# Performance work log

Measured on AMD Instinct MI355X. Metric: run time of the kernel, lower is better.

## Reference

```python
import jax, jax.numpy as jnp
import numpy as np

B, H, SEQLEN, HEAD_DIM = 1, 16, 4096, 64
SCALE = 1.0 / float(np.sqrt(HEAD_DIM))


def setup_inputs() -> dict:
    key = jax.random.key(0)
    kq, kk, kv = jax.random.split(key, 3)
    q = jax.random.normal(kq, (B, H, SEQLEN, HEAD_DIM), dtype=jnp.float32)
    k = jax.random.normal(kk, (B, H, HEAD_DIM, SEQLEN), dtype=jnp.float32)  # pre-transposed
    v = jax.random.normal(kv, (B, H, SEQLEN, HEAD_DIM), dtype=jnp.float32)
    return {"q": q, "k": k, "v": v}


def reference(q, k, v):
    # causal additive mask: -inf strictly above the diagonal
    mask = jnp.where(
        jnp.triu(jnp.ones((SEQLEN, SEQLEN), dtype=bool), k=1),
        jnp.float32(-jnp.inf), jnp.float32(0.0),
    ).astype(q.dtype)
    scores = jnp.einsum('bhsd,bhdt->bhst', q, k) * SCALE + mask  # [B,H,S,S]
    row_max = jnp.max(scores, axis=-1, keepdims=True)
    p_exp = jnp.exp(scores - row_max)
    denom = jnp.sum(p_exp, axis=-1, keepdims=True)
    p = p_exp / denom                                            # softmax probs
    out = jnp.einsum('bhst,bhtd->bhsd', p, v)                    # [B,H,S,D]
    row_sum = jnp.sum(p, axis=2)                                 # per-key accumulated attention [B,H,S]
    return (out, row_sum)
```

## Files before the change

### kernel.cpp

```cpp
#include <hip/hip_runtime.h>
#include <hip/hip_bf16.h>

#define HEADS 16
#define SEQ   4096
#define DIM   64
#define QT    64
#define KT    64
#define SCALE 0.125f
#define CF    0.18033688011112042f
#define LOG2E 1.4426950408889634f

typedef __bf16 v8bf  __attribute__((ext_vector_type(8)));
typedef __bf16 v4bf  __attribute__((ext_vector_type(4)));
typedef float  f32x4 __attribute__((ext_vector_type(4)));

__device__ __forceinline__ __bf16 to_bf(float f) { return (__bf16)f; }
__device__ __forceinline__ float ex2(float x) { return __builtin_amdgcn_exp2f(x); }
__device__ __forceinline__ float lg2(float x) { return __builtin_amdgcn_logf(x); }

__device__ __forceinline__ void gload16(const __bf16* g, __bf16* l) {
    __builtin_amdgcn_global_load_lds(
        (const __attribute__((address_space(1))) void*)g,
        (__attribute__((address_space(3))) void*)l,
        16, 0, 0);
}

__global__ __launch_bounds__(256) void conv_q_kernel(
    const float* __restrict__ qg, __bf16* __restrict__ Qb)
{
    size_t i = ((size_t)blockIdx.x * 256 + threadIdx.x) * 8;
    float4 f0 = *(const float4*)(qg + i);
    float4 f1 = *(const float4*)(qg + i + 4);
    v8bf o;
    o[0] = to_bf(f0.x * CF); o[1] = to_bf(f0.y * CF);
    o[2] = to_bf(f0.z * CF); o[3] = to_bf(f0.w * CF);
    o[4] = to_bf(f1.x * CF); o[5] = to_bf(f1.y * CF);
    o[6] = to_bf(f1.z * CF); o[7] = to_bf(f1.w * CF);
    *(v8bf*)(Qb + i) = o;
}

__global__ __launch_bounds__(256) void conv_kv_kernel(
    const float* __restrict__ kg, const float* __restrict__ vg,
    __bf16* __restrict__ Kb, __bf16* __restrict__ Vb)
{
    __shared__ __bf16 ldsT[64][65];
    const int h   = blockIdx.y;
    const int t0  = blockIdx.x * 64;
    const int tid = threadIdx.x;
    const int rr  = tid >> 2;
    const int cq  = (tid & 3) * 16;

    if (blockIdx.z == 0) {
        const float* src = kg + ((size_t)h * DIM + rr) * SEQ + t0 + cq;
        #pragma unroll
        for (int j = 0; j < 4; ++j) {
            float4 f = *(const float4*)(src + 4 * j);
            ldsT[rr][cq + 4 * j + 0] = to_bf(f.x);
            ldsT[rr][cq + 4 * j + 1] = to_bf(f.y);
            ldsT[rr][cq + 4 * j + 2] = to_bf(f.z);
            ldsT[rr][cq + 4 * j + 3] = to_bf(f.w);
        }
        __syncthreads();
        __bf16* dst = Kb + (size_t)h * SEQ * DIM + (size_t)(t0 + rr) * DIM + cq;
        v8bf o0, o1;
        #pragma unroll
        for (int i = 0; i < 8; ++i) {
            o0[i] = ldsT[cq + i][rr];
            o1[i] = ldsT[cq + 8 + i][rr];
        }
        *(v8bf*)dst = o0;
        *(v8bf*)(dst + 8) = o1;
    } else {
        const float* src = vg + ((size_t)h * SEQ + t0 + rr) * DIM + cq;
        #pragma unroll
        for (int j = 0; j < 4; ++j) {
            float4 f = *(const float4*)(src + 4 * j);
            ldsT[rr][cq + 4 * j + 0] = to_bf(f.x);
            ldsT[rr][cq + 4 * j + 1] = to_bf(f.y);
            ldsT[rr][cq + 4 * j + 2] = to_bf(f.z);
            ldsT[rr][cq + 4 * j + 3] = to_bf(f.w);
        }
        __syncthreads();
        __bf16* dst0 = Vb + ((size_t)h * DIM + rr) * SEQ + t0;
        const int n  = cq >> 4;
        const int c0 = 32 * (n >> 1) + 4 * (n & 1);
        #pragma unroll
        for (int j2 = 0; j2 < 4; ++j2) {
            v4bf ch;
            #pragma unroll
            for (int r = 0; r < 4; ++r)
                ch[r] = ldsT[cq + 4 * j2 + r][rr];
            *(v4bf*)(dst0 + c0 + 8 * j2) = ch;
        }
    }
}

__global__ __launch_bounds__(256, 2) void fa_fwd2_kernel(
    const __bf16* __restrict__ Qb, const __bf16* __restrict__ Kb,
    const __bf16* __restrict__ Vb, float* __restrict__ outg,
    float* __restrict__ lseg)
{
    const int b    = blockIdx.x;
    const int xcd  = b & 7;
    const int j    = b >> 3;
    const int h    = 2 * xcd + (j & 1);
    const int bq   = j >> 1;
    const int tid  = threadIdx.x;
    const int wave = tid >> 6;
    const int lane = tid & 63;
    const int g    = lane >> 4;
    const int l16  = lane & 15;

    __shared__ alignas(16) __bf16 ldsK[2][KT * DIM];
    __shared__ alignas(16) __bf16 ldsV[2][DIM * KT];

    const int r0 = tid >> 3;
    const int c0 = tid & 7;
    const size_t kOff0 = (size_t)r0 * DIM + (size_t)((c0 ^ (r0 & 7)) << 3);
    const size_t kOff1 = (size_t)(r0 + 32) * DIM + (size_t)((c0 ^ ((r0 + 32) & 7)) << 3);
    const size_t vOff0 = (size_t)r0 * SEQ + (size_t)((c0 ^ (r0 & 7)) << 3);
    const size_t vOff1 = (size_t)(r0 + 32) * SEQ + (size_t)((c0 ^ ((r0 + 32) & 7)) << 3);
    const __bf16* KbH = Kb + (size_t)h * SEQ * DIM;
    const __bf16* VbH = Vb + (size_t)h * DIM * SEQ;
    const int ldsW = wave * 512;

    #pragma unroll 1
    for (int pi = 0; pi < 2; ++pi) {
        const int qtile = pi ? (63 - bq) : bq;
        const int qw = qtile * QT + wave * 16;
        const int nt = qtile + 1;
        const int q  = qw + l16;

        const __bf16* qrow = Qb + ((size_t)h * SEQ + q) * DIM + g * 8;
        v8bf aq0 = *(const v8bf*)qrow;
        v8bf aq1 = *(const v8bf*)(qrow + 32);

        f32x4 acc[4];
        #pragma unroll
        for (int n = 0; n < 4; ++n) acc[n] = (f32x4){0.f, 0.f, 0.f, 0.f};
        float lp[4] = {0.f, 0.f, 0.f, 0.f};

        int cur = 0;
        gload16(KbH + kOff0, &ldsK[0][ldsW]);
        gload16(KbH + kOff1, &ldsK[0][2048 + ldsW]);
        gload16(VbH + vOff0, &ldsV[0][ldsW]);
        gload16(VbH + vOff1, &ldsV[0][2048 + ldsW]);
        __syncthreads();

        #pragma unroll 1
        for (int t = 0; t < nt; ++t) {
            if (t + 1 < nt) {
                const size_t kt = (size_t)(t + 1) * KT * DIM;
                const size_t vt = (size_t)(t + 1) * KT;
                gload16(KbH + kt + kOff0, &ldsK[cur ^ 1][ldsW]);
                gload16(KbH + kt + kOff1, &ldsK[cur ^ 1][2048 + ldsW]);
                gload16(VbH + vt + vOff0, &ldsV[cur ^ 1][ldsW]);
                gload16(VbH + vt + vOff1, &ldsV[cur ^ 1][2048 + ldsW]);
            }
            f32x4 s[4];
            #pragma unroll
            for (int n = 0; n < 4; ++n) s[n] = (f32x4){0.f, 0.f, 0.f, 0.f};
            __builtin_amdgcn_s_setprio(1);
            #pragma unroll
            for (int kk = 0; kk < 2; ++kk) {
                #pragma unroll
                for (int n = 0; n < 4; ++n) {
                    int row  = 16 * n + l16;
                    int byte = row * 128 + kk * 64 + g * 16;
                    byte ^= (row & 7) << 4;
                    v8bf ak = *(const v8bf*)&ldsK[cur][byte >> 1];
                    s[n] = __builtin_amdgcn_mfma_f32_16x16x32_bf16(
                        ak, kk ? aq1 : aq0, s[n], 0, 0, 0);
                }
            }
            __builtin_amdgcn_s_setprio(0);
            if (t == nt - 1) {
                const int qit = wave * 16 + l16;
                #pragma unroll
                for (int n = 0; n < 4; ++n)
                    #pragma unroll
                    for (int r = 0; r < 4; ++r)
                        if (16 * n + 4 * g + r > qit) s[n][r] = -3.0e38f;
            }
            v8bf pa0, pa1;
            #pragma unroll
            for (int n = 0; n < 4; ++n) {
                #pragma unroll
                for (int r = 0; r < 4; ++r) {
                    float p = ex2(s[n][r]);
                    lp[r] += p;
                    if (n < 2) pa0[(n & 1) * 4 + r] = to_bf(p);
                    else       pa1[(n & 1) * 4 + r] = to_bf(p);
                }
            }
            __builtin_amdgcn_s_setprio(1);
            #pragma unroll
            for (int kk = 0; kk < 2; ++kk) {
                #pragma unroll
                for (int n = 0; n < 4; ++n) {
                    int row  = 16 * n + l16;
                    int byte = row * 128 + kk * 64 + g * 16;
                    byte ^= (row & 7) << 4;
                    v8bf av = *(const v8bf*)&ldsV[cur][byte >> 1];
                    acc[n] = __builtin_amdgcn_mfma_f32_16x16x32_bf16(
                        av, kk ? pa1 : pa0, acc[n], 0, 0, 0);
                }
            }
            __builtin_amdgcn_s_setprio(0);
            __syncthreads();
            cur ^= 1;
        }

        float l = (lp[0] + lp[1]) + (lp[2] + lp[3]);
        l += __shfl_xor(l, 16);
        l += __shfl_xor(l, 32);
        const float inv = 1.0f / l;
        float* orow = outg + ((size_t)h * SEQ + q) * DIM;
        #pragma unroll
        for (int n = 0; n < 4; ++n) {
            f32x4 o = acc[n];
            o[0] *= inv; o[1] *= inv; o[2] *= inv; o[3] *= inv;
            *(f32x4*)(orow + 16 * n + 4 * g) = o;
        }
        if (g == 0)
            lseg[h * SEQ + q] = lg2(l);
    }
}

__global__ __launch_bounds__(256, 2) void fa_colsum2_kernel(
    const __bf16* __restrict__ Qb, const __bf16* __restrict__ Kb,
    const float* __restrict__ lseg, float* __restrict__ rsg)
{
    const int b    = blockIdx.x;
    const int xcd  = b & 7;
    const int j    = b >> 3;
    const int h    = 2 * xcd + (j & 1);
    const int ta   = j >> 1;
    const int tb   = 63 - ta;
    const int tid  = threadIdx.x;
    const int wave = tid >> 6;
    const int lane = tid & 63;
    const int g    = lane >> 4;
    const int l16  = lane & 15;

    __shared__ alignas(16) __bf16 ldsK2[2][KT * DIM];
    __shared__ float cs[2][4][KT];

    const int r0 = tid >> 3;
    const int c0 = tid & 7;
    const size_t kOff0 = (size_t)r0 * DIM + (size_t)((c0 ^ (r0 & 7)) << 3);
    const size_t kOff1 = (size_t)(r0 + 32) * DIM + (size_t)((c0 ^ ((r0 + 32) & 7)) << 3);
    const __bf16* KbH = Kb + (size_t)h * SEQ * DIM;
    const int ldsW = wave * 512;

    gload16(KbH + (size_t)ta * KT * DIM + kOff0, &ldsK2[0][ldsW]);
    gload16(KbH + (size_t)ta * KT * DIM + kOff1, &ldsK2[0][2048 + ldsW]);
    gload16(KbH + (size_t)tb * KT * DIM + kOff0, &ldsK2[1][ldsW]);
    gload16(KbH + (size_t)tb * KT * DIM + kOff1, &ldsK2[1][2048 + ldsW]);
    __syncthreads();

    float accA[4] = {0.f, 0.f, 0.f, 0.f};
    float accB[4] = {0.f, 0.f, 0.f, 0.f};

    #pragma unroll 1
    for (int qt = ta; qt < SEQ / QT; ++qt) {
        const int qw = qt * QT + wave * 16;
        const __bf16* qrow = Qb + ((size_t)h * SEQ + qw + l16) * DIM + g * 8;
        v8bf aq0 = *(const v8bf*)qrow;
        v8bf aq1 = *(const v8bf*)(qrow + 32);
        float4 lse4 = *(const float4*)(lseg + (size_t)h * SEQ + qw + 4 * g);

        {
            f32x4 s[4];
            #pragma unroll
            for (int n = 0; n < 4; ++n) s[n] = (f32x4){0.f, 0.f, 0.f, 0.f};
            __builtin_amdgcn_s_setprio(1);
            #pragma unroll
            for (int kk = 0; kk < 2; ++kk)
                #pragma unroll
                for (int n = 0; n < 4; ++n) {
                    int row  = 16 * n + l16;
                    int byte = row * 128 + kk * 64 + g * 16;
                    byte ^= (row & 7) << 4;
                    v8bf bk = *(const v8bf*)&ldsK2[0][byte >> 1];
                    s[n] = __builtin_amdgcn_mfma_f32_16x16x32_bf16(
                        kk ? aq1 : aq0, bk, s[n], 0, 0, 0);
                }
            __builtin_amdgcn_s_setprio(0);
            if (qt == ta) {
                #pragma unroll
                for (int n = 0; n < 4; ++n) {
                    const int key = ta * KT + 16 * n + l16;
                    #pragma unroll
                    for (int r = 0; r < 4; ++r) {
                        float e = ex2(s[n][r] - lse4[r]);
                        accA[n] += (key <= qw + 4 * g + r) ? e : 0.f;
                    }
                }
            } else {
                #pragma unroll
                for (int n = 0; n < 4; ++n)
                    #pragma unroll
                    for (int r = 0; r < 4; ++r)
                        accA[n] += ex2(s[n][r] - lse4[r]);
            }
        }
        if (qt >= tb) {
            f32x4 s[4];
            #pragma unroll
            for (int n = 0; n < 4; ++n) s[n] = (f32x4){0.f, 0.f, 0.f, 0.f};
            __builtin_amdgcn_s_setprio(1);
            #pragma unroll
            for (int kk = 0; kk < 2; ++kk)
                #pragma unroll
                for (int n = 0; n < 4; ++n) {
                    int row  = 16 * n + l16;
                    int byte = row * 128 + kk * 64 + g * 16;
                    byte ^= (row & 7) << 4;
                    v8bf bk = *(const v8bf*)&ldsK2[1][byte >> 1];
                    s[n] = __builtin_amdgcn_mfma_f32_16x16x32_bf16(
                        kk ? aq1 : aq0, bk, s[n], 0, 0, 0);
                }
            __builtin_amdgcn_s_setprio(0);
            if (qt == tb) {
                #pragma unroll
                for (int n = 0; n < 4; ++n) {
                    const int key = tb * KT + 16 * n + l16;
                    #pragma unroll
                    for (int r = 0; r < 4; ++r) {
                        float e = ex2(s[n][r] - lse4[r]);
                        accB[n] += (key <= qw + 4 * g + r) ? e : 0.f;
                    }
                }
            } else {
                #pragma unroll
                for (int n = 0; n < 4; ++n)
                    #pragma unroll
                    for (int r = 0; r < 4; ++r)
                        accB[n] += ex2(s[n][r] - lse4[r]);
            }
        }
    }

    #pragma unroll
    for (int n = 0; n < 4; ++n) {
        accA[n] += __shfl_xor(accA[n], 16);
        accA[n] += __shfl_xor(accA[n], 32);
        accB[n] += __shfl_xor(accB[n], 16);
        accB[n] += __shfl_xor(accB[n], 32);
    }
    if (lane < 16) {
        #pragma unroll
        for (int n = 0; n < 4; ++n) {
            cs[0][wave][16 * n + lane] = accA[n];
            cs[1][wave][16 * n + lane] = accB[n];
        }
    }
    __syncthreads();
    if (tid < KT) {
        rsg[(size_t)h * SEQ + ta * KT + tid] =
            cs[0][0][tid] + cs[0][1][tid] + cs[0][2][tid] + cs[0][3][tid];
    } else if (tid < 2 * KT) {
        const int t = tid - KT;
        rsg[(size_t)h * SEQ + tb * KT + t] =
            cs[1][0][t] + cs[1][1][t] + cs[1][2][t] + cs[1][3][t];
    }
}

__global__ __launch_bounds__(256, 1) void fa_fwd_v1_kernel(
    const float* __restrict__ qg, const float* __restrict__ kg,
    const float* __restrict__ vg, float* __restrict__ outg,
    float* __restrict__ lseg)
{
    const int h    = blockIdx.y;
    const int q0   = blockIdx.x * QT;
    const int tid  = threadIdx.x;
    const int wave = tid >> 6;
    const int lane = tid & 63;
    const int g    = lane >> 4;
    const int l16  = lane & 15;

    __shared__ alignas(16) __bf16 ldsK[KT * DIM];
    __shared__ alignas(16) __bf16 ldsV[DIM * KT];
    __shared__ alignas(16) __bf16 ldsP[4][16 * 72];

    const int qw = q0 + wave * 16;
    v8bf aq[2];
    {
        const float* qrow = qg + ((size_t)h * SEQ + qw + l16) * DIM;
        #pragma unroll
        for (int kk = 0; kk < 2; ++kk) {
            const float* p = qrow + kk * 32 + g * 8;
            float4 f0 = *(const float4*)p;
            float4 f1 = *(const float4*)(p + 4);
            aq[kk][0] = to_bf(f0.x); aq[kk][1] = to_bf(f0.y);
            aq[kk][2] = to_bf(f0.z); aq[kk][3] = to_bf(f0.w);
            aq[kk][4] = to_bf(f1.x); aq[kk][5] = to_bf(f1.y);
            aq[kk][6] = to_bf(f1.z); aq[kk][7] = to_bf(f1.w);
        }
    }
    f32x4 acc[4];
    #pragma unroll
    for (int n = 0; n < 4; ++n) acc[n] = (f32x4){0.f, 0.f, 0.f, 0.f};
    float m_r[4], l_r[4];
    #pragma unroll
    for (int r = 0; r < 4; ++r) { m_r[r] = -__builtin_inff(); l_r[r] = 0.f; }

    const int ntiles = q0 / KT + 1;
    const int kd = tid >> 2;
    const int kc = (tid & 3) * 16;

    for (int t = 0; t < ntiles; ++t) {
        const int t0 = t * KT;
        __syncthreads();
        {
            const float* src = kg + ((size_t)h * DIM + kd) * SEQ + t0 + kc;
            #pragma unroll
            for (int j = 0; j < 4; ++j) {
                float4 f = *(const float4*)(src + 4 * j);
                #pragma unroll
                for (int i = 0; i < 4; ++i) {
                    int row  = kc + 4 * j + i;
                    int byte = row * 128 + kd * 2;
                    byte ^= (row & 7) << 4;
                    ldsK[byte >> 1] = to_bf(((const float*)&f)[i]);
                }
            }
        }
        {
            const float* src = vg + ((size_t)h * SEQ + t0 + kd) * DIM + kc;
            #pragma unroll
            for (int j = 0; j < 4; ++j) {
                float4 f = *(const float4*)(src + 4 * j);
                #pragma unroll
                for (int i = 0; i < 4; ++i) {
                    int row  = kc + 4 * j + i;
                    int byte = row * 128 + kd * 2;
                    byte ^= (row & 7) << 4;
                    ldsV[byte >> 1] = to_bf(((const float*)&f)[i]);
                }
            }
        }
        __syncthreads();

        f32x4 s[4];
        #pragma unroll
        for (int n = 0; n < 4; ++n) s[n] = (f32x4){0.f, 0.f, 0.f, 0.f};
        #pragma unroll
        for (int kk = 0; kk < 2; ++kk)
            #pragma unroll
            for (int n = 0; n < 4; ++n) {
                int row  = 16 * n + l16;
                int byte = row * 128 + kk * 64 + g * 16;
                byte ^= (row & 7) << 4;
                v8bf bk = *(const v8bf*)&ldsK[byte >> 1];
                s[n] = __builtin_amdgcn_mfma_f32_16x16x32_bf16(aq[kk], bk, s[n], 0, 0, 0);
            }
        float pvv[4][4];
        #pragma unroll
        for (int r = 0; r < 4; ++r) {
            const int qq = qw + 4 * g + r;
            float sv[4];
            #pragma unroll
            for (int n = 0; n < 4; ++n) {
                int key = t0 + 16 * n + l16;
                sv[n] = (key <= qq) ? s[n][r] * (SCALE * LOG2E) : -3.0e38f;
            }
            float mx = fmaxf(fmaxf(sv[0], sv[1]), fmaxf(sv[2], sv[3]));
            mx = fmaxf(mx, __shfl_xor(mx, 1));
            mx = fmaxf(mx, __shfl_xor(mx, 2));
            mx = fmaxf(mx, __shfl_xor(mx, 4));
            mx = fmaxf(mx, __shfl_xor(mx, 8));
            float mnew = fmaxf(m_r[r], mx);
            float corr = ex2(m_r[r] - mnew);
            m_r[r] = mnew;
            float rs = 0.f;
            #pragma unroll
            for (int n = 0; n < 4; ++n) {
                float p = (sv[n] > -1.0e38f) ? ex2(sv[n] - mnew) : 0.f;
                pvv[n][r] = p;
                rs += p;
            }
            rs += __shfl_xor(rs, 1);
            rs += __shfl_xor(rs, 2);
            rs += __shfl_xor(rs, 4);
            rs += __shfl_xor(rs, 8);
            l_r[r] = l_r[r] * corr + rs;
            #pragma unroll
            for (int n = 0; n < 4; ++n) acc[n][r] *= corr;
        }
        #pragma unroll
        for (int n = 0; n < 4; ++n)
            #pragma unroll
            for (int r = 0; r < 4; ++r)
                ldsP[wave][(4 * g + r) * 72 + 16 * n + l16] = to_bf(pvv[n][r]);
        asm volatile("s_waitcnt lgkmcnt(0)" ::: "memory");
        __builtin_amdgcn_sched_barrier(0);
        #pragma unroll
        for (int kk = 0; kk < 2; ++kk) {
            v8bf ap = *(const v8bf*)&ldsP[wave][l16 * 72 + 32 * kk + 8 * g];
            #pragma unroll
            for (int n = 0; n < 4; ++n) {
                int row  = 16 * n + l16;
                int byte = row * 128 + kk * 64 + g * 16;
                byte ^= (row & 7) << 4;
                v8bf bv = *(const v8bf*)&ldsV[byte >> 1];
                acc[n] = __builtin_amdgcn_mfma_f32_16x16x32_bf16(ap, bv, acc[n], 0, 0, 0);
            }
        }
    }
    #pragma unroll
    for (int r = 0; r < 4; ++r) {
        const int qq  = qw + 4 * g + r;
        const float inv = 1.0f / l_r[r];
        float* orow = outg + ((size_t)h * SEQ + qq) * DIM;
        #pragma unroll
        for (int n = 0; n < 4; ++n)
            orow[16 * n + l16] = acc[n][r] * inv;
        if (l16 == 0)
            lseg[h * SEQ + qq] = m_r[r] + lg2(l_r[r]);
    }
}

__global__ __launch_bounds__(256, 1) void fa_colsum_v1_kernel(
    const float* __restrict__ qg, const float* __restrict__ kg,
    const float* __restrict__ lseg, float* __restrict__ rsg)
{
    const int h    = blockIdx.y;
    const int t0   = blockIdx.x * KT;
    const int tid  = threadIdx.x;
    const int wave = tid >> 6;
    const int lane = tid & 63;
    const int g    = lane >> 4;
    const int l16  = lane & 15;

    __shared__ alignas(16) __bf16 ldsK[KT * DIM];
    __shared__ float cs[4][KT];
    {
        const int kd = tid >> 2;
        const int kc = (tid & 3) * 16;
        const float* src = kg + ((size_t)h * DIM + kd) * SEQ + t0 + kc;
        #pragma unroll
        for (int j = 0; j < 4; ++j) {
            float4 f = *(const float4*)(src + 4 * j);
            #pragma unroll
            for (int i = 0; i < 4; ++i) {
                int row  = kc + 4 * j + i;
                int byte = row * 128 + kd * 2;
                byte ^= (row & 7) << 4;
                ldsK[byte >> 1] = to_bf(((const float*)&f)[i]);
            }
        }
    }
    __syncthreads();
    float colacc[4] = {0.f, 0.f, 0.f, 0.f};
    for (int qt = t0 / QT; qt < SEQ / QT; ++qt) {
        const int qw = qt * QT + wave * 16;
        const float* qrow = qg + ((size_t)h * SEQ + qw + l16) * DIM;
        v8bf aq[2];
        #pragma unroll
        for (int kk = 0; kk < 2; ++kk) {
            const float* p = qrow + kk * 32 + g * 8;
            float4 f0 = *(const float4*)p;
            float4 f1 = *(const float4*)(p + 4);
            aq[kk][0] = to_bf(f0.x); aq[kk][1] = to_bf(f0.y);
            aq[kk][2] = to_bf(f0.z); aq[kk][3] = to_bf(f0.w);
            aq[kk][4] = to_bf(f1.x); aq[kk][5] = to_bf(f1.y);
            aq[kk][6] = to_bf(f1.z); aq[kk][7] = to_bf(f1.w);
        }
        float lse_r[4];
        #pragma unroll
        for (int r = 0; r < 4; ++r)
            lse_r[r] = lseg[h * SEQ + qw + 4 * g + r];
        f32x4 s[4];
        #pragma unroll
        for (int n = 0; n < 4; ++n) s[n] = (f32x4){0.f, 0.f, 0.f, 0.f};
        #pragma unroll
        for (int kk = 0; kk < 2; ++kk)
            #pragma unroll
            for (int n = 0; n < 4; ++n) {
                int row  = 16 * n + l16;
                int byte = row * 128 + kk * 64 + g * 16;
                byte ^= (row & 7) << 4;
                v8bf bk = *(const v8bf*)&ldsK[byte >> 1];
                s[n] = __builtin_amdgcn_mfma_f32_16x16x32_bf16(aq[kk], bk, s[n], 0, 0, 0);
            }
        #pragma unroll
        for (int n = 0; n < 4; ++n) {
            const int key = t0 + 16 * n + l16;
            #pragma unroll
            for (int r = 0; r < 4; ++r) {
                const int qq = qw + 4 * g + r;
                if (key <= qq)
                    colacc[n] += ex2(s[n][r] * (SCALE * LOG2E) - lse_r[r]);
            }
        }
    }
    #pragma unroll
    for (int n = 0; n < 4; ++n) {
        colacc[n] += __shfl_xor(colacc[n], 16);
        colacc[n] += __shfl_xor(colacc[n], 32);
    }
    if (lane < 16) {
        #pragma unroll
        for (int n = 0; n < 4; ++n)
            cs[wave][16 * n + lane] = colacc[n];
    }
    __syncthreads();
    if (tid < KT) {
        float v = cs[0][tid] + cs[1][tid] + cs[2][tid] + cs[3][tid];
        rsg[h * SEQ + t0 + tid] = v;
    }
}

extern "C" void kernel_launch(void* const* d_in, const int* in_sizes, int n_in,
                              void* d_out, int out_size, void* d_ws, size_t ws_size,
                              hipStream_t stream) {
    (void)in_sizes; (void)n_in; (void)out_size;
    const float* qg = (const float*)d_in[0];
    const float* kg = (const float*)d_in[1];
    const float* vg = (const float*)d_in[2];
    float* outg = (float*)d_out;
    float* rsg  = outg + (size_t)HEADS * SEQ * DIM;

    const size_t nElem   = (size_t)HEADS * SEQ * DIM;
    const size_t lseB    = (size_t)HEADS * SEQ * sizeof(float);
    const size_t needB   = lseB + 3 * nElem * sizeof(__bf16);

    if (ws_size >= needB) {
        float*  lseg = (float*)d_ws;
        __bf16* Qb = (__bf16*)((char*)d_ws + lseB);
        __bf16* Kb = Qb + nElem;
        __bf16* Vb = Kb + nElem;
        conv_q_kernel<<<dim3((int)(nElem / 2048)), 256, 0, stream>>>(qg, Qb);
        conv_kv_kernel<<<dim3(SEQ / 64, HEADS, 2), 256, 0, stream>>>(kg, vg, Kb, Vb);
        fa_fwd2_kernel<<<dim3(512), 256, 0, stream>>>(Qb, Kb, Vb, outg, lseg);
        fa_colsum2_kernel<<<dim3(512), 256, 0, stream>>>(Qb, Kb, lseg, rsg);
    } else {
        float* lseg = (float*)d_ws;
        dim3 grid(SEQ / QT, HEADS);
        fa_fwd_v1_kernel<<<grid, 256, 0, stream>>>(qg, kg, vg, outg, lseg);
        fa_colsum_v1_kernel<<<grid, 256, 0, stream>>>(qg, kg, lseg, rsg);
    }
}
```

Measured before the change: 117.8 us.

## Process two 64-key KV tiles per loop iteration in forward attention

Each main-loop iteration of the forward kernel now loads and consumes two 64-wide K/V tiles (128 keys) instead of one. The LDS buffers gain an extra dimension to match. This halves the number of barriers and loop trips and gives the scheduler two independent MFMA chains to interleave. In exchange it doubles LDS use per block and adds register pressure. When the tile count is odd, the last iteration also computes a fully masked extra tile, which is wasted work.

Result: faster. 105.3 us (-10.6%).

```diff
diff --git a/kernel.cpp b/kernel.cpp
--- a/kernel.cpp
+++ b/kernel.cpp
@@ -111,8 +111,8 @@
     const int g    = lane >> 4;
     const int l16  = lane & 15;
 
-    __shared__ alignas(16) __bf16 ldsK[2][KT * DIM];
-    __shared__ alignas(16) __bf16 ldsV[2][DIM * KT];
+    __shared__ alignas(16) __bf16 ldsK[2][2][KT * DIM];
+    __shared__ alignas(16) __bf16 ldsV[2][2][DIM * KT];
 
     const int r0 = tid >> 3;
     const int c0 = tid & 7;
@@ -128,8 +128,9 @@
     for (int pi = 0; pi < 2; ++pi) {
         const int qtile = pi ? (63 - bq) : bq;
         const int qw = qtile * QT + wave * 16;
-        const int nt = qtile + 1;
-        const int q  = qw + l16;
+        const int nt  = qtile + 1;
+        const int nIt = (nt + 1) >> 1;
+        const int q   = qw + l16;
 
         const __bf16* qrow = Qb + ((size_t)h * SEQ + q) * DIM + g * 8;
         v8bf aq0 = *(const v8bf*)qrow;
@@ -141,25 +142,36 @@
         float lp[4] = {0.f, 0.f, 0.f, 0.f};
 
         int cur = 0;
-        gload16(KbH + kOff0, &ldsK[0][ldsW]);
-        gload16(KbH + kOff1, &ldsK[0][2048 + ldsW]);
-        gload16(VbH + vOff0, &ldsV[0][ldsW]);
-        gload16(VbH + vOff1, &ldsV[0][2048 + ldsW]);
+        #pragma unroll
+        for (int u = 0; u < 2; ++u) {
+            const __bf16* kb = KbH + (size_t)(64 * u) * DIM;
+            const __bf16* vb = VbH + 64 * u;
+            gload16(kb + kOff0, &ldsK[0][u][ldsW]);
+            gload16(kb + kOff1, &ldsK[0][u][2048 + ldsW]);
+            gload16(vb + vOff0, &ldsV[0][u][ldsW]);
+            gload16(vb + vOff1, &ldsV[0][u][2048 + ldsW]);
+        }
         __syncthreads();
 
         #pragma unroll 1
-        for (int t = 0; t < nt; ++t) {
-            if (t + 1 < nt) {
-                const size_t kt = (size_t)(t + 1) * KT * DIM;
-                const size_t vt = (size_t)(t + 1) * KT;
-                gload16(KbH + kt + kOff0, &ldsK[cur ^ 1][ldsW]);
-                gload16(KbH + kt + kOff1, &ldsK[cur ^ 1][2048 + ldsW]);
-                gload16(VbH + vt + vOff0, &ldsV[cur ^ 1][ldsW]);
-                gload16(VbH + vt + vOff1, &ldsV[cur ^ 1][2048 + ldsW]);
-            }
-            f32x4 s[4];
-            #pragma unroll
-            for (int n = 0; n < 4; ++n) s[n] = (f32x4){0.f, 0.f, 0.f, 0.f};
+        for (int it = 0; it < nIt; ++it) {
+            if (it + 1 < nIt) {
+                #pragma unroll
+                for (int u = 0; u < 2; ++u) {
+                    const __bf16* kb = KbH + (size_t)(128 * (it + 1) + 64 * u) * DIM;
+                    const __bf16* vb = VbH + 128 * (it + 1) + 64 * u;
+                    gload16(kb + kOff0, &ldsK[cur ^ 1][u][ldsW]);
+                    gload16(kb + kOff1, &ldsK[cur ^ 1][u][2048 + ldsW]);
+                    gload16(vb + vOff0, &ldsV[cur ^ 1][u][ldsW]);
+                    gload16(vb + vOff1, &ldsV[cur ^ 1][u][2048 + ldsW]);
+                }
+            }
+            f32x4 s0[4], s1[4];
+            #pragma unroll
+            for (int n = 0; n < 4; ++n) {
+                s0[n] = (f32x4){0.f, 0.f, 0.f, 0.f};
+                s1[n] = (f32x4){0.f, 0.f, 0.f, 0.f};
+            }
             __builtin_amdgcn_s_setprio(1);
             #pragma unroll
             for (int kk = 0; kk < 2; ++kk) {
@@ -168,29 +180,44 @@
                     int row  = 16 * n + l16;
                     int byte = row * 128 + kk * 64 + g * 16;
                     byte ^= (row & 7) << 4;
-                    v8bf ak = *(const v8bf*)&ldsK[cur][byte >> 1];
-                    s[n] = __builtin_amdgcn_mfma_f32_16x16x32_bf16(
-                        ak, kk ? aq1 : aq0, s[n], 0, 0, 0);
+                    v8bf ak0 = *(const v8bf*)&ldsK[cur][0][byte >> 1];
+                    v8bf ak1 = *(const v8bf*)&ldsK[cur][1][byte >> 1];
+                    s0[n] = __builtin_amdgcn_mfma_f32_16x16x32_bf16(
+                        ak0, kk ? aq1 : aq0, s0[n], 0, 0, 0);
+                    s1[n] = __builtin_amdgcn_mfma_f32_16x16x32_bf16(
+                        ak1, kk ? aq1 : aq0, s1[n], 0, 0, 0);
                 }
             }
             __builtin_amdgcn_s_setprio(0);
-            if (t == nt - 1) {
-                const int qit = wave * 16 + l16;
+            const int st0 = 2 * it, st1 = 2 * it + 1;
+            if (st0 >= nt - 1) {
+                const int lim = (qtile - st0) * 64 + wave * 16 + l16;
                 #pragma unroll
                 for (int n = 0; n < 4; ++n)
                     #pragma unroll
                     for (int r = 0; r < 4; ++r)
-                        if (16 * n + 4 * g + r > qit) s[n][r] = -3.0e38f;
-            }
-            v8bf pa0, pa1;
+                        if (16 * n + 4 * g + r > lim) s0[n][r] = -3.0e38f;
+            }
+            if (st1 >= nt - 1) {
+                const int lim = (qtile - st1) * 64 + wave * 16 + l16;
+                #pragma unroll
+                for (int n = 0; n < 4; ++n)
+                    #pragma unroll
+                    for (int r = 0; r < 4; ++r)
+                        if (16 * n + 4 * g + r > lim) s1[n][r] = -3.0e38f;
+            }
+            v8bf pa00, pa01, pa10, pa11;
             #pragma unroll
             for (int n = 0; n < 4; ++n) {
                 #pragma unroll
                 for (int r = 0; r < 4; ++r) {
-                    float p = ex2(s[n][r]);
-                    lp[r] += p;
-                    if (n < 2) pa0[(n & 1) * 4 + r] = to_bf(p);
-                    else       pa1[(n & 1) * 4 + r] = to_bf(p);
+                    float p0 = ex2(s0[n][r]);
+                    float p1 = ex2(s1[n][r]);
+                    lp[r] += p0 + p1;
+                    if (n < 2) { pa00[(n & 1) * 4 + r] = to_bf(p0);
+                                 pa10[(n & 1) * 4 + r] = to_bf(p1); }
+                    else       { pa01[(n & 1) * 4 + r] = to_bf(p0);
+                                 pa11[(n & 1) * 4 + r] = to_bf(p1); }
                 }
             }
             __builtin_amdgcn_s_setprio(1);
@@ -201,9 +228,12 @@
                     int row  = 16 * n + l16;
                     int byte = row * 128 + kk * 64 + g * 16;
                     byte ^= (row & 7) << 4;
-                    v8bf av = *(const v8bf*)&ldsV[cur][byte >> 1];
+                    v8bf av0 = *(const v8bf*)&ldsV[cur][0][byte >> 1];
+                    v8bf av1 = *(const v8bf*)&ldsV[cur][1][byte >> 1];
                     acc[n] = __builtin_amdgcn_mfma_f32_16x16x32_bf16(
-                        av, kk ? pa1 : pa0, acc[n], 0, 0, 0);
+                        av0, kk ? pa01 : pa00, acc[n], 0, 0, 0);
+                    acc[n] = __builtin_amdgcn_mfma_f32_16x16x32_bf16(
+                        av1, kk ? pa11 : pa10, acc[n], 0, 0, 0);
                 }
             }
             __builtin_amdgcn_s_setprio(0);
```

## Split attention and column-sum work across more blocks with longest-first scheduling

Applied to the files above, without the earlier changes.

The forward kernel now runs one query tile per block (1024 blocks, heaviest tiles first) instead of pairing two tiles per block. The column-sum kernel splits each key-tile pair's query range into two halves at a balance point, writes partial sums to a scratch buffer that reuses the V workspace after the forward pass, and a new small kernel adds the two partials. Launch bounds are raised to 4 blocks per SM. The goal is more parallelism and better load balance on the causal triangle, at the cost of an extra kernel launch and partial-sum traffic.

Measured after the change: 113.6 us. -3.6%, faster.

```diff
diff --git a/kernel.cpp b/kernel.cpp
--- a/kernel.cpp
+++ b/kernel.cpp
@@ -95,21 +95,21 @@
     }
 }
 
-__global__ __launch_bounds__(256, 2) void fa_fwd2_kernel(
+__global__ __launch_bounds__(256, 4) void fa_fwd3_kernel(
     const __bf16* __restrict__ Qb, const __bf16* __restrict__ Kb,
     const __bf16* __restrict__ Vb, float* __restrict__ outg,
     float* __restrict__ lseg)
 {
-    const int b    = blockIdx.x;
-    const int xcd  = b & 7;
-    const int j    = b >> 3;
-    const int h    = 2 * xcd + (j & 1);
-    const int bq   = j >> 1;
-    const int tid  = threadIdx.x;
-    const int wave = tid >> 6;
-    const int lane = tid & 63;
-    const int g    = lane >> 4;
-    const int l16  = lane & 15;
+    const int b     = blockIdx.x;
+    const int xcd   = b & 7;
+    const int r     = b >> 3;
+    const int h     = 2 * xcd + (r & 1);
+    const int qtile = 63 - (r >> 1);
+    const int tid   = threadIdx.x;
+    const int wave  = tid >> 6;
+    const int lane  = tid & 63;
+    const int g     = lane >> 4;
+    const int l16   = lane & 15;
 
     __shared__ alignas(16) __bf16 ldsK[2][KT * DIM];
     __shared__ alignas(16) __bf16 ldsV[2][DIM * KT];
@@ -124,119 +124,120 @@
     const __bf16* VbH = Vb + (size_t)h * DIM * SEQ;
     const int ldsW = wave * 512;
 
+    const int qw = qtile * QT + wave * 16;
+    const int nt = qtile + 1;
+    const int q  = qw + l16;
+
+    const __bf16* qrow = Qb + ((size_t)h * SEQ + q) * DIM + g * 8;
+    v8bf aq0 = *(const v8bf*)qrow;
+    v8bf aq1 = *(const v8bf*)(qrow + 32);
+
+    f32x4 acc[4];
+    #pragma unroll
+    for (int n = 0; n < 4; ++n) acc[n] = (f32x4){0.f, 0.f, 0.f, 0.f};
+    float lp[4] = {0.f, 0.f, 0.f, 0.f};
+
+    int cur = 0;
+    gload16(KbH + kOff0, &ldsK[0][ldsW]);
+    gload16(KbH + kOff1, &ldsK[0][2048 + ldsW]);
+    gload16(VbH + vOff0, &ldsV[0][ldsW]);
+    gload16(VbH + vOff1, &ldsV[0][2048 + ldsW]);
+    __syncthreads();
+
     #pragma unroll 1
-    for (int pi = 0; pi < 2; ++pi) {
-        const int qtile = pi ? (63 - bq) : bq;
-        const int qw = qtile * QT + wave * 16;
-        const int nt = qtile + 1;
-        const int q  = qw + l16;
-
-        const __bf16* qrow = Qb + ((size_t)h * SEQ + q) * DIM + g * 8;
-        v8bf aq0 = *(const v8bf*)qrow;
-        v8bf aq1 = *(const v8bf*)(qrow + 32);
-
-        f32x4 acc[4];
-        #pragma unroll
-        for (int n = 0; n < 4; ++n) acc[n] = (f32x4){0.f, 0.f, 0.f, 0.f};
-        float lp[4] = {0.f, 0.f, 0.f, 0.f};
-
-        int cur = 0;
-        gload16(KbH + kOff0, &ldsK[0][ldsW]);
-        gload16(KbH + kOff1, &ldsK[0][2048 + ldsW]);
-        gload16(VbH + vOff0, &ldsV[0][ldsW]);
-        gload16(VbH + vOff1, &ldsV[0][2048 + ldsW]);
+    for (int t = 0; t < nt; ++t) {
+        if (t + 1 < nt) {
+            const size_t kt = (size_t)(t + 1) * KT * DIM;
+            const size_t vt = (size_t)(t + 1) * KT;
+            gload16(KbH + kt + kOff0, &ldsK[cur ^ 1][ldsW]);
+            gload16(KbH + kt + kOff1, &ldsK[cur ^ 1][2048 + ldsW]);
+            gload16(VbH + vt + vOff0, &ldsV[cur ^ 1][ldsW]);
+            gload16(VbH + vt + vOff1, &ldsV[cur ^ 1][2048 + ldsW]);
+        }
+        f32x4 s[4];
+        #pragma unroll
+        for (int n = 0; n < 4; ++n) s[n] = (f32x4){0.f, 0.f, 0.f, 0.f};
+        __builtin_amdgcn_s_setprio(1);
+        #pragma unroll
+        for (int kk = 0; kk < 2; ++kk) {
+            #pragma unroll
+            for (int n = 0; n < 4; ++n) {
+                int row  = 16 * n + l16;
+                int byte = row * 128 + kk * 64 + g * 16;
+                byte ^= (row & 7) << 4;
+                v8bf ak = *(const v8bf*)&ldsK[cur][byte >> 1];
+                s[n] = __builtin_amdgcn_mfma_f32_16x16x32_bf16(
+                    ak, kk ? aq1 : aq0, s[n], 0, 0, 0);
+            }
+        }
+        __builtin_amdgcn_s_setprio(0);
+        if (t == nt - 1) {
+            const int qit = wave * 16 + l16;
+            #pragma unroll
+            for (int n = 0; n < 4; ++n)
+                #pragma unroll
+                for (int r2 = 0; r2 < 4; ++r2)
+                    if (16 * n + 4 * g + r2 > qit) s[n][r2] = -3.0e38f;
+        }
+        v8bf pa0, pa1;
+        #pragma unroll
+        for (int n = 0; n < 4; ++n) {
+            #pragma unroll
+            for (int r2 = 0; r2 < 4; ++r2) {
+                float p = ex2(s[n][r2]);
+                lp[r2] += p;
+                if (n < 2) pa0[(n & 1) * 4 + r2] = to_bf(p);
+                else       pa1[(n & 1) * 4 + r2] = to_bf(p);
+            }
+        }
+        __builtin_amdgcn_s_setprio(1);
+        #pragma unroll
+        for (int kk = 0; kk < 2; ++kk) {
+            #pragma unroll
+            for (int n = 0; n < 4; ++n) {
+                int row  = 16 * n + l16;
+                int byte = row * 128 + kk * 64 + g * 16;
+                byte ^= (row & 7) << 4;
+                v8bf av = *(const v8bf*)&ldsV[cur][byte >> 1];
+                acc[n] = __builtin_amdgcn_mfma_f32_16x16x32_bf16(
+                    av, kk ? pa1 : pa0, acc[n], 0, 0, 0);
+            }
+        }
+        __builtin_amdgcn_s_setprio(0);
         __syncthreads();
-
-        #pragma unroll 1
-        for (int t = 0; t < nt; ++t) {
-            if (t + 1 < nt) {
-                const size_t kt = (size_t)(t + 1) * KT * DIM;
-                const size_t vt = (size_t)(t + 1) * KT;
-                gload16(KbH + kt + kOff0, &ldsK[cur ^ 1][ldsW]);
-                gload16(KbH + kt + kOff1, &ldsK[cur ^ 1][2048 + ldsW]);
-                gload16(VbH + vt + vOff0, &ldsV[cur ^ 1][ldsW]);
-                gload16(VbH + vt + vOff1, &ldsV[cur ^ 1][2048 + ldsW]);
-            }
-            f32x4 s[4];
-            #pragma unroll
-            for (int n = 0; n < 4; ++n) s[n] = (f32x4){0.f, 0.f, 0.f, 0.f};
-            __builtin_amdgcn_s_setprio(1);
-            #pragma unroll
-            for (int kk = 0; kk < 2; ++kk) {
-                #pragma unroll
-                for (int n = 0; n < 4; ++n) {
-                    int row  = 16 * n + l16;
-                    int byte = row * 128 + kk * 64 + g * 16;
-                    byte ^= (row & 7) << 4;
-                    v8bf ak = *(const v8bf*)&ldsK[cur][byte >> 1];
-                    s[n] = __builtin_amdgcn_mfma_f32_16x16x32_bf16(
-                        ak, kk ? aq1 : aq0, s[n], 0, 0, 0);
-                }
-            }
-            __builtin_amdgcn_s_setprio(0);
-            if (t == nt - 1) {
-                const int qit = wave * 16 + l16;
-                #pragma unroll
-                for (int n = 0; n < 4; ++n)
-                    #pragma unroll
-                    for (int r = 0; r < 4; ++r)
-                        if (16 * n + 4 * g + r > qit) s[n][r] = -3.0e38f;
-            }
-            v8bf pa0, pa1;
-            #pragma unroll
-            for (int n = 0; n < 4; ++n) {
-                #pragma unroll
-                for (int r = 0; r < 4; ++r) {
-                    float p = ex2(s[n][r]);
-                    lp[r] += p;
-                    if (n < 2) pa0[(n & 1) * 4 + r] = to_bf(p);
-                    else       pa1[(n & 1) * 4 + r] = to_bf(p);
-                }
-            }
-            __builtin_amdgcn_s_setprio(1);
-            #pragma unroll
-            for (int kk = 0; kk < 2; ++kk) {
-                #pragma unroll
-                for (int n = 0; n < 4; ++n) {
-                    int row  = 16 * n + l16;
-                    int byte = row * 128 + kk * 64 + g * 16;
-                    byte ^= (row & 7) << 4;
-                    v8bf av = *(const v8bf*)&ldsV[cur][byte >> 1];
-                    acc[n] = __builtin_amdgcn_mfma_f32_16x16x32_bf16(
-                        av, kk ? pa1 : pa0, acc[n], 0, 0, 0);
-                }
-            }
-            __builtin_amdgcn_s_setprio(0);
-            __syncthreads();
-            cur ^= 1;
-        }
-
-        float l = (lp[0] + lp[1]) + (lp[2] + lp[3]);
-        l += __shfl_xor(l, 16);
-        l += __shfl_xor(l, 32);
-        const float inv = 1.0f / l;
-        float* orow = outg + ((size_t)h * SEQ + q) * DIM;
-        #pragma unroll
-        for (int n = 0; n < 4; ++n) {
-            f32x4 o = acc[n];
-            o[0] *= inv; o[1] *= inv; o[2] *= inv; o[3] *= inv;
-            *(f32x4*)(orow + 16 * n + 4 * g) = o;
-        }
-        if (g == 0)
-            lseg[h * SEQ + q] = lg2(l);
-    }
-}
-
-__global__ __launch_bounds__(256, 2) void fa_colsum2_kernel(
+        cur ^= 1;
+    }
+
+    float l = (lp[0] + lp[1]) + (lp[2] + lp[3]);
+    l += __shfl_xor(l, 16);
+    l += __shfl_xor(l, 32);
+    const float inv = 1.0f / l;
+    float* orow = outg + ((size_t)h * SEQ + q) * DIM;
+    #pragma unroll
+    for (int n = 0; n < 4; ++n) {
+        f32x4 o = acc[n];
+        o[0] *= inv; o[1] *= inv; o[2] *= inv; o[3] *= inv;
+        *(f32x4*)(orow + 16 * n + 4 * g) = o;
+    }
+    if (g == 0)
+        lseg[h * SEQ + q] = lg2(l);
+}
+
+__global__ __launch_bounds__(256, 4) void fa_colsum2_kernel(
     const __bf16* __restrict__ Qb, const __bf16* __restrict__ Kb,
-    const float* __restrict__ lseg, float* __restrict__ rsg)
+    const float* __restrict__ lseg, float* __restrict__ partg)
 {
     const int b    = blockIdx.x;
     const int xcd  = b & 7;
     const int j    = b >> 3;
     const int h    = 2 * xcd + (j & 1);
-    const int ta   = j >> 1;
+    const int m    = j >> 1;
+    const int ta   = m & 31;
+    const int half = m >> 5;
     const int tb   = 63 - ta;
+    const int smid = (ta <= 15) ? (ta + 33) : 48;
+    const int qlo  = half ? smid : ta;
+    const int qhiE = half ? 64 : smid;
     const int tid  = threadIdx.x;
     const int wave = tid >> 6;
     const int lane = tid & 63;
@@ -263,7 +264,7 @@
     float accB[4] = {0.f, 0.f, 0.f, 0.f};
 
     #pragma unroll 1
-    for (int qt = ta; qt < SEQ / QT; ++qt) {
+    for (int qt = qlo; qt < qhiE; ++qt) {
         const int qw = qt * QT + wave * 16;
         const __bf16* qrow = Qb + ((size_t)h * SEQ + qw + l16) * DIM + g * 8;
         v8bf aq0 = *(const v8bf*)qrow;
@@ -292,17 +293,17 @@
                 for (int n = 0; n < 4; ++n) {
                     const int key = ta * KT + 16 * n + l16;
                     #pragma unroll
-                    for (int r = 0; r < 4; ++r) {
-                        float e = ex2(s[n][r] - lse4[r]);
-                        accA[n] += (key <= qw + 4 * g + r) ? e : 0.f;
+                    for (int r2 = 0; r2 < 4; ++r2) {
+                        float e = ex2(s[n][r2] - lse4[r2]);
+                        accA[n] += (key <= qw + 4 * g + r2) ? e : 0.f;
                     }
                 }
             } else {
                 #pragma unroll
                 for (int n = 0; n < 4; ++n)
                     #pragma unroll
-                    for (int r = 0; r < 4; ++r)
-                        accA[n] += ex2(s[n][r] - lse4[r]);
+                    for (int r2 = 0; r2 < 4; ++r2)
+                        accA[n] += ex2(s[n][r2] - lse4[r2]);
             }
         }
         if (qt >= tb) {
@@ -327,17 +328,17 @@
                 for (int n = 0; n < 4; ++n) {
                     const int key = tb * KT + 16 * n + l16;
                     #pragma unroll
-                    for (int r = 0; r < 4; ++r) {
-                        float e = ex2(s[n][r] - lse4[r]);
-                        accB[n] += (key <= qw + 4 * g + r) ? e : 0.f;
+                    for (int r2 = 0; r2 < 4; ++r2) {
+                        float e = ex2(s[n][r2] - lse4[r2]);
+                        accB[n] += (key <= qw + 4 * g + r2) ? e : 0.f;
                     }
                 }
             } else {
                 #pragma unroll
                 for (int n = 0; n < 4; ++n)
                     #pragma unroll
-                    for (int r = 0; r < 4; ++r)
-                        accB[n] += ex2(s[n][r] - lse4[r]);
+                    for (int r2 = 0; r2 < 4; ++r2)
+                        accB[n] += ex2(s[n][r2] - lse4[r2]);
             }
         }
     }
@@ -357,14 +358,25 @@
         }
     }
     __syncthreads();
+    float* pg = partg + (size_t)half * HEADS * SEQ + (size_t)h * SEQ;
     if (tid < KT) {
-        rsg[(size_t)h * SEQ + ta * KT + tid] =
+        pg[ta * KT + tid] =
             cs[0][0][tid] + cs[0][1][tid] + cs[0][2][tid] + cs[0][3][tid];
     } else if (tid < 2 * KT) {
         const int t = tid - KT;
-        rsg[(size_t)h * SEQ + tb * KT + t] =
+        pg[tb * KT + t] =
             cs[1][0][t] + cs[1][1][t] + cs[1][2][t] + cs[1][3][t];
     }
+}
+
+__global__ __launch_bounds__(256) void rs_add_kernel(
+    const float* __restrict__ partg, float* __restrict__ rsg)
+{
+    const int i = blockIdx.x * 256 + threadIdx.x;
+    f32x4 x = *(const f32x4*)(partg + (size_t)i * 4);
+    f32x4 y = *(const f32x4*)(partg + (size_t)HEADS * SEQ + (size_t)i * 4);
+    x[0] += y[0]; x[1] += y[1]; x[2] += y[2]; x[3] += y[3];
+    *(f32x4*)(rsg + (size_t)i * 4) = x;
 }
 
 __global__ __launch_bounds__(256, 1) void fa_fwd_v1_kernel(
@@ -632,10 +644,12 @@
         __bf16* Qb = (__bf16*)((char*)d_ws + lseB);
         __bf16* Kb = Qb + nElem;
         __bf16* Vb = Kb + nElem;
+        float* partg = (float*)Vb;
         conv_q_kernel<<<dim3((int)(nElem / 2048)), 256, 0, stream>>>(qg, Qb);
         conv_kv_kernel<<<dim3(SEQ / 64, HEADS, 2), 256, 0, stream>>>(kg, vg, Kb, Vb);
-        fa_fwd2_kernel<<<dim3(512), 256, 0, stream>>>(Qb, Kb, Vb, outg, lseg);
-        fa_colsum2_kernel<<<dim3(512), 256, 0, stream>>>(Qb, Kb, lseg, rsg);
+        fa_fwd3_kernel<<<dim3(1024), 256, 0, stream>>>(Qb, Kb, Vb, outg, lseg);
+        fa_colsum2_kernel<<<dim3(1024), 256, 0, stream>>>(Qb, Kb, lseg, partg);
+        rs_add_kernel<<<dim3(HEADS * SEQ / 1024), 256, 0, stream>>>(partg, rsg);
     } else {
         float* lseg = (float*)d_ws;
         dim3 grid(SEQ / QT, HEADS);
```
